# Optimization experiments

Hardware: AMD Instinct MI355X
Metric: run time of the kernel (lower is better)

Reference implementation:

```python
import jax, jax.numpy as jnp
import numpy as np

D = 1024
H = 16
DK = D // H
SCALE = 1.0 / jnp.sqrt(jnp.float32(DK))


def setup_inputs() -> dict:
    key0 = jax.random.key(0)
    ks = jax.random.split(key0, 11)
    B, S = 2, 2048
    std = 1.0 / np.sqrt(D)
    inp = {
        "query": jax.random.normal(ks[0], (B, S, D), jnp.float32),
        "key": jax.random.normal(ks[1], (B, S, D), jnp.float32),
        "value": jax.random.normal(ks[2], (B, S, D), jnp.float32),
        "wq": jax.random.normal(ks[3], (D, D), jnp.float32) * std,
        "bq": jax.random.normal(ks[4], (D,), jnp.float32) * std,
        "wk": jax.random.normal(ks[5], (D, D), jnp.float32) * std,
        "bk": jax.random.normal(ks[6], (D,), jnp.float32) * std,
        "wv": jax.random.normal(ks[7], (D, D), jnp.float32) * std,
        "bv": jax.random.normal(ks[8], (D,), jnp.float32) * std,
        "wo": jax.random.normal(ks[9], (D, D), jnp.float32) * std,
        "bo": jax.random.normal(ks[10], (D,), jnp.float32) * std,
    }
    return inp


def _split_heads(x):
    # [B,S,D] -> [B,H,S,dk]
    B, S, _ = x.shape
    return x.reshape(B, S, H, DK).transpose(0, 2, 1, 3)


def reference(query, key, value, wq, bq, wk, bk, wv, bv, wo, bo):
    B, S, _ = query.shape
    # Linear projections (torch nn.Linear: x @ W^T + b)
    q = _split_heads(query @ wq.T + bq)
    k = _split_heads(key @ wk.T + bk)
    v = _split_heads(value @ wv.T + bv)
    # Scaled dot-product attention scores [B,H,S,S]
    scores = jnp.einsum("bhqd,bhkd->bhqk", q * SCALE, k)
    attention = jax.nn.softmax(scores, axis=-1)
    # Dropout in eval mode == identity
    out = jnp.einsum("bhqk,bhkd->bhqd", attention, v)
    out = out.transpose(0, 2, 1, 3).reshape(B, S, D)
    out = out @ wo.T + bo
    return out, attention
```

## Files before the change

### kernel.cpp

```cpp
#include <hip/hip_runtime.h>
#include <stdint.h>

typedef __attribute__((ext_vector_type(4))) float f32x4;
typedef __attribute__((ext_vector_type(8))) short short8;
typedef __attribute__((ext_vector_type(2))) unsigned int u32x2;

#define MFMA16(a, b, c) __builtin_amdgcn_mfma_f32_16x16x32_bf16((a), (b), (c), 0, 0, 0)
#define EXP2(x) __builtin_amdgcn_exp2f(x)
#define LOG2(x) __builtin_amdgcn_logf(x)

__device__ __forceinline__ unsigned short f2bf(float f) {
  unsigned int x = __float_as_uint(f);
  return (unsigned short)((x + 0x7fffu + ((x >> 16) & 1u)) >> 16);
}

__device__ __forceinline__ unsigned int cvtpk(float lo, float hi) {
  unsigned int d;
  asm("v_cvt_pk_bf16_f32 %0, %1, %2" : "=v"(d) : "v"(lo), "v"(hi));
  return d;
}

__device__ __forceinline__ void gl2lds16(const void* g, void* l) {
  __builtin_amdgcn_global_load_lds((const __attribute__((address_space(1))) void*)g,
                                   (__attribute__((address_space(3))) void*)l, 16, 0, 0);
}

__device__ __forceinline__ void load8cv(const float* __restrict__ s, void* d) {
  const f32x4* p = (const f32x4*)s;
  f32x4 a = p[0], b = p[1];
  short8 t;
  t[0] = (short)f2bf(a[0]); t[1] = (short)f2bf(a[1]);
  t[2] = (short)f2bf(a[2]); t[3] = (short)f2bf(a[3]);
  t[4] = (short)f2bf(b[0]); t[5] = (short)f2bf(b[1]);
  t[6] = (short)f2bf(b[2]); t[7] = (short)f2bf(b[3]);
  *(short8*)d = t;
}

#define BAR_V4 asm volatile("s_waitcnt vmcnt(4)\ns_barrier" ::: "memory")
#define BAR_V8 asm volatile("s_waitcnt vmcnt(8)\ns_barrier" ::: "memory")
#define BAR_V0 asm volatile("s_waitcnt vmcnt(0)\ns_barrier" ::: "memory")
#define BAR_RAW asm volatile("s_barrier" ::: "memory")

__global__ __launch_bounds__(256) void cast_weights(const float* __restrict__ wq,
                                                    const float* __restrict__ wk,
                                                    const float* __restrict__ wv,
                                                    const float* __restrict__ wo,
                                                    unsigned short* __restrict__ dst) {
  int i = blockIdx.x * 256 + threadIdx.x;
  int which = i >> 17;
  int off = (i & 131071) * 8;
  const float* src = which == 0 ? wq : which == 1 ? wk : which == 2 ? wv : wo;
  load8cv(src + off, dst + (size_t)which * 1048576 + off);
}

__global__ __launch_bounds__(256) void qkv_proj(const float* __restrict__ q_in,
                                                const float* __restrict__ k_in,
                                                const float* __restrict__ v_in,
                                                const unsigned short* __restrict__ W16,
                                                const float* __restrict__ bq,
                                                const float* __restrict__ bk,
                                                const float* __restrict__ bv,
                                                unsigned short* __restrict__ Q16,
                                                unsigned short* __restrict__ K16,
                                                unsigned short* __restrict__ V16) {
  const int z = blockIdx.z;
  const float* A = z == 0 ? q_in : z == 1 ? k_in : v_in;
  const unsigned short* Bt = W16 + (size_t)z * 1048576;
  const float* bias = z == 0 ? bq : z == 1 ? bk : bv;
  unsigned short* C = z == 0 ? Q16 : z == 1 ? K16 : V16;
  const float oscale = z == 0 ? 0.18033688f : 1.0f;
  const int K = 1024, N = 1024;

  __shared__ __align__(16) char lds[32768];
  char* As = lds;
  char* Bs = lds + 16384;
  const int tid = threadIdx.x;
  const int lane = tid & 63;
  const int wv = tid >> 6;
  const int g = lane >> 4, r = lane & 15;
  const int wm = wv >> 1, wn = wv & 1;
  const int m0 = blockIdx.y * 128, n0 = blockIdx.x * 128;

  f32x4 acc[4][4];
#pragma unroll
  for (int m = 0; m < 4; ++m)
#pragma unroll
    for (int n = 0; n < 4; ++n) acc[m][n] = (f32x4){0.f, 0.f, 0.f, 0.f};

  for (int k0 = 0; k0 < K; k0 += 64) {
    __syncthreads();
#pragma unroll
    for (int i = 0; i < 4; ++i) {
      int c = (wv * 4 + i) * 64 + lane;
      int row = c >> 3;
      gl2lds16(Bt + (size_t)(n0 + row) * K + k0 + (c & 7) * 8, Bs + (wv * 4 + i) * 1024);
    }
#pragma unroll
    for (int i = 0; i < 4; ++i) {
      int c = tid + i * 256;
      int row = c >> 3, e = (c & 7) * 8;
      load8cv(A + (size_t)(m0 + row) * K + k0 + e, As + c * 16);
    }
    __syncthreads();
#pragma unroll
    for (int kk = 0; kk < 2; ++kk) {
      short8 af[4], bfr[4];
#pragma unroll
      for (int m = 0; m < 4; ++m)
        af[m] = *(const short8*)(As + (wm * 64 + m * 16 + r) * 128 + kk * 64 + g * 16);
#pragma unroll
      for (int n = 0; n < 4; ++n)
        bfr[n] = *(const short8*)(Bs + (wn * 64 + n * 16 + r) * 128 + kk * 64 + g * 16);
#pragma unroll
      for (int m = 0; m < 4; ++m)
#pragma unroll
        for (int n = 0; n < 4; ++n) acc[m][n] = MFMA16(af[m], bfr[n], acc[m][n]);
    }
  }

#pragma unroll
  for (int n = 0; n < 4; ++n) {
    int col = n0 + wn * 64 + n * 16 + r;
    float bv_ = bias[col];
#pragma unroll
    for (int m = 0; m < 4; ++m)
#pragma unroll
      for (int i = 0; i < 4; ++i) {
        int rowg = m0 + wm * 64 + m * 16 + 4 * g + i;
        C[(size_t)rowg * N + col] = f2bf((acc[m][n][i] + bv_) * oscale);
      }
  }
}

__global__ __launch_bounds__(256) void o_proj(const unsigned short* __restrict__ A,
                                              const unsigned short* __restrict__ Bt,
                                              const float* __restrict__ bias,
                                              float* __restrict__ C) {
  const int K = 1024, N = 1024;
  __shared__ __align__(16) char lds[24576];
  char* As = lds;
  char* Bs = lds + 16384;
  const int tid = threadIdx.x;
  const int lane = tid & 63;
  const int wv = tid >> 6;
  const int g = lane >> 4, r = lane & 15;
  const int wm = wv >> 1, wn = wv & 1;
  const int m0 = blockIdx.y * 128, n0 = blockIdx.x * 64;

  f32x4 acc[4][2];
#pragma unroll
  for (int m = 0; m < 4; ++m)
#pragma unroll
    for (int n = 0; n < 2; ++n) acc[m][n] = (f32x4){0.f, 0.f, 0.f, 0.f};

  for (int k0 = 0; k0 < K; k0 += 64) {
    __syncthreads();
#pragma unroll
    for (int i = 0; i < 2; ++i) {
      int c = (wv * 2 + i) * 64 + lane;
      int row = c >> 3;
      gl2lds16(Bt + (size_t)(n0 + row) * K + k0 + (c & 7) * 8, Bs + (wv * 2 + i) * 1024);
    }
#pragma unroll
    for (int i = 0; i < 4; ++i) {
      int c = (wv * 4 + i) * 64 + lane;
      int row = c >> 3;
      gl2lds16(A + (size_t)(m0 + row) * K + k0 + (c & 7) * 8, As + (wv * 4 + i) * 1024);
    }
    __syncthreads();
#pragma unroll
    for (int kk = 0; kk < 2; ++kk) {
      short8 af[4], bfr[2];
#pragma unroll
      for (int m = 0; m < 4; ++m)
        af[m] = *(const short8*)(As + (wm * 64 + m * 16 + r) * 128 + kk * 64 + g * 16);
#pragma unroll
      for (int n = 0; n < 2; ++n)
        bfr[n] = *(const short8*)(Bs + (wn * 32 + n * 16 + r) * 128 + kk * 64 + g * 16);
#pragma unroll
      for (int m = 0; m < 4; ++m)
#pragma unroll
        for (int n = 0; n < 2; ++n) acc[m][n] = MFMA16(af[m], bfr[n], acc[m][n]);
    }
  }

#pragma unroll
  for (int n = 0; n < 2; ++n) {
    int col = n0 + wn * 32 + n * 16 + r;
    float bv_ = bias[col];
#pragma unroll
    for (int m = 0; m < 4; ++m)
#pragma unroll
      for (int i = 0; i < 4; ++i) {
        int rowg = m0 + wm * 64 + m * 16 + 4 * g + i;
        C[(size_t)rowg * N + col] = acc[m][n][i] + bv_;
      }
  }
}

__global__ __launch_bounds__(256) void transpose_v(const unsigned short* __restrict__ V,
                                                   unsigned short* __restrict__ Vt) {
  int t = blockIdx.x * 256 + threadIdx.x;
  int d = t & 63;
  int sc = (t >> 6) & 255;
  int bh = t >> 14;
  int b = bh >> 4, h = bh & 15;
  unsigned short vals[8];
#pragma unroll
  for (int j = 0; j < 8; ++j)
    vals[j] = V[(size_t)(b * 2048 + sc * 8 + j) * 1024 + h * 64 + d];
  *(short8*)&Vt[((size_t)bh * 64 + d) * 2048 + sc * 8] = *(short8*)vals;
}

__global__ __launch_bounds__(256, 4) void attn_fused(const unsigned short* __restrict__ Q,
                                                     const unsigned short* __restrict__ K,
                                                     const unsigned short* __restrict__ Vt,
                                                     float* __restrict__ attn,
                                                     unsigned short* __restrict__ O) {
  __shared__ __align__(16) char lds[32768];
  const int tid = threadIdx.x;
  const int lane = tid & 63;
  const int wv = tid >> 6;
  const int g = lane >> 4, r = lane & 15;
  int nb = (blockIdx.x & 7) * 128 + (blockIdx.x >> 3);
  const int qt = nb & 31, bh = nb >> 5, h = bh & 15, b = bh >> 4;
  const int qloc = qt * 64 + wv * 16;
  const int qrow0 = b * 2048 + qloc;
  const unsigned short* Kbh = K + (size_t)b * 2048 * 1024 + h * 64;
  const unsigned short* Vbh = Vt + (size_t)bh * 64 * 2048;
  float* attn_bh = attn + (size_t)bh * 2048 * 2048;

  short8 qf[2];
#pragma unroll
  for (int kk = 0; kk < 2; ++kk)
    qf[kk] = *(const short8*)&Q[(size_t)(qrow0 + r) * 1024 + h * 64 + kk * 32 + g * 8];

#define P1_ISSUE(bb, ktt)                                                      \
  do {                                                                         \
    _Pragma("unroll") for (int i_ = 0; i_ < 4; ++i_) {                         \
      int c_ = (wv * 4 + i_) * 64 + lane;                                      \
      int kr_ = c_ >> 3;                                                       \
      int scb_ = ((c_ & 7) * 16) ^ ((kr_ & 7) << 4);                           \
      gl2lds16(Kbh + (size_t)((ktt) + kr_) * 1024 + (scb_ >> 1),               \
               (bb) + (wv * 4 + i_) * 1024);                                   \
    }                                                                          \
  } while (0)
#define P2_ISSUE(bb, ktt)                                                      \
  do {                                                                         \
    _Pragma("unroll") for (int i_ = 0; i_ < 4; ++i_) {                         \
      int c_ = (wv * 4 + i_) * 64 + lane;                                      \
      int kr_ = (c_ >> 3) & 63;                                                \
      int scb_ = ((c_ & 7) * 16) ^ ((kr_ & 7) << 4);                           \
      const unsigned short* src_ =                                             \
          (c_ < 512) ? (Kbh + (size_t)((ktt) + kr_) * 1024 + (scb_ >> 1))      \
                     : (Vbh + (size_t)kr_ * 2048 + (ktt) + (scb_ >> 1));       \
      gl2lds16(src_, (bb) + (wv * 4 + i_) * 1024);                             \
    }                                                                          \
  } while (0)

  float lrow = 0.f;
  int cur = 0;
  P1_ISSUE(lds, 0);
  for (int t = 0; t < 16; ++t) {
    char* bcur = lds + (cur << 14);
    char* bnxt = lds + ((cur ^ 1) << 14);
    if (t < 15) {
      P1_ISSUE(bnxt, (t + 1) * 128);
      BAR_V4;
    } else {
      BAR_V0;
    }
#pragma unroll
    for (int ct = 0; ct < 8; ++ct) {
      int row = ct * 16 + r;
      int sw = (row & 7) << 4;
      short8 kf0 = *(const short8*)(bcur + ((row * 128 + g * 16) ^ sw));
      short8 kf1 = *(const short8*)(bcur + ((row * 128 + 64 + g * 16) ^ sw));
      f32x4 s = (f32x4){0.f, 0.f, 0.f, 0.f};
      s = MFMA16(kf0, qf[0], s);
      s = MFMA16(kf1, qf[1], s);
      lrow += (EXP2(s[0]) + EXP2(s[1])) + (EXP2(s[2]) + EXP2(s[3]));
    }
    BAR_RAW;
    cur ^= 1;
  }
  lrow += __shfl_xor(lrow, 16);
  lrow += __shfl_xor(lrow, 32);
  const float negml = -LOG2(lrow);
  const f32x4 cinit = (f32x4){negml, negml, negml, negml};

  f32x4 oacc[4];
#pragma unroll
  for (int i = 0; i < 4; ++i) oacc[i] = (f32x4){0.f, 0.f, 0.f, 0.f};

  float* arow = attn_bh + (size_t)(qloc + r) * 2048 + 4 * g;
  cur = 0;
  P2_ISSUE(lds, 0);
  for (int t = 0; t < 32; ++t) {
    char* bcur = lds + (cur << 14);
    char* bnxt = lds + ((cur ^ 1) << 14);
    int kt = t * 64;
    if (t < 31) {
      P2_ISSUE(bnxt, kt + 64);
      if (t == 0) {
        BAR_V4;
      } else {
        BAR_V8;
      }
    } else {
      BAR_V0;
    }
    unsigned w[4][2];
#pragma unroll
    for (int ct = 0; ct < 4; ++ct) {
      int row = ct * 16 + r;
      int sw = (row & 7) << 4;
      short8 kf0 = *(const short8*)(bcur + ((row * 128 + g * 16) ^ sw));
      short8 kf1 = *(const short8*)(bcur + ((row * 128 + 64 + g * 16) ^ sw));
      f32x4 s = MFMA16(kf0, qf[0], cinit);
      s = MFMA16(kf1, qf[1], s);
      f32x4 p;
      p[0] = EXP2(s[0]); p[1] = EXP2(s[1]);
      p[2] = EXP2(s[2]); p[3] = EXP2(s[3]);
      __builtin_nontemporal_store(p, (f32x4*)(arow + kt + 16 * ct));
      w[ct][0] = cvtpk(p[0], p[1]);
      w[ct][1] = cvtpk(p[2], p[3]);
    }
    __builtin_amdgcn_s_setprio(1);
#pragma unroll
    for (int kk2 = 0; kk2 < 2; ++kk2) {
      unsigned x0 = w[2 * kk2][0], y0 = w[2 * kk2 + 1][0];
      unsigned x1 = w[2 * kk2][1], y1 = w[2 * kk2 + 1][1];
      asm("v_permlane32_swap_b32 %0, %1" : "+v"(x0), "+v"(y0));
      asm("v_permlane16_swap_b32 %0, %1" : "+v"(x0), "+v"(y0));
      asm("v_permlane32_swap_b32 %0, %1" : "+v"(x1), "+v"(y1));
      asm("v_permlane16_swap_b32 %0, %1" : "+v"(x1), "+v"(y1));
      union { unsigned u[4]; short8 v8; } pau;
      pau.u[0] = x0; pau.u[1] = x1; pau.u[2] = y0; pau.u[3] = y1;
      short8 pa = pau.v8;
#pragma unroll
      for (int ct2 = 0; ct2 < 4; ++ct2) {
        int vrow = ct2 * 16 + r;
        short8 vf = *(const short8*)(bcur + 8192 +
                                     ((vrow * 128 + kk2 * 64 + g * 16) ^ ((vrow & 7) << 4)));
        oacc[ct2] = MFMA16(pa, vf, oacc[ct2]);
      }
    }
    __builtin_amdgcn_s_setprio(0);
    BAR_RAW;
    cur ^= 1;
  }
#pragma unroll
  for (int ct2 = 0; ct2 < 4; ++ct2)
#pragma unroll
    for (int i = 0; i < 4; ++i)
      O[(size_t)(qrow0 + 4 * g + i) * 1024 + h * 64 + ct2 * 16 + r] = f2bf(oacc[ct2][i]);
#undef P1_ISSUE
#undef P2_ISSUE
}

extern "C" void kernel_launch(void* const* d_in, const int* in_sizes, int n_in,
                              void* d_out, int out_size, void* d_ws, size_t ws_size,
                              hipStream_t stream) {
  const float* q_in = (const float*)d_in[0];
  const float* k_in = (const float*)d_in[1];
  const float* v_in = (const float*)d_in[2];
  const float* wq = (const float*)d_in[3];
  const float* bq = (const float*)d_in[4];
  const float* wk = (const float*)d_in[5];
  const float* bk = (const float*)d_in[6];
  const float* wv = (const float*)d_in[7];
  const float* bv = (const float*)d_in[8];
  const float* wo = (const float*)d_in[9];
  const float* bo = (const float*)d_in[10];

  char* ws = (char*)d_ws;
  const size_t MB8 = 8ull * 1024 * 1024;
  unsigned short* W16 = (unsigned short*)(ws);
  unsigned short* Q16 = (unsigned short*)(ws + MB8);
  unsigned short* K16 = (unsigned short*)(ws + 2 * MB8);
  unsigned short* V16 = (unsigned short*)(ws + 3 * MB8);
  unsigned short* Vt  = (unsigned short*)(ws + 4 * MB8);
  unsigned short* O16 = (unsigned short*)(ws + 3 * MB8);

  float* out = (float*)d_out;
  float* attn = out + 4194304ull;

  dim3 blk(256);
  cast_weights<<<dim3(2048), blk, 0, stream>>>(wq, wk, wv, wo, W16);
  qkv_proj<<<dim3(8, 32, 3), blk, 0, stream>>>(q_in, k_in, v_in, W16, bq, bk, bv, Q16, K16, V16);
  transpose_v<<<dim3(2048), blk, 0, stream>>>(V16, Vt);
  attn_fused<<<dim3(1024), blk, 0, stream>>>(Q16, K16, Vt, attn, O16);
  o_proj<<<dim3(16, 32), blk, 0, stream>>>(O16, W16 + 3145728, bo, out);
}
```

Measured before the change: 290.3 us.

## Pre-cast activations to bf16 and restructure attention loop barriers

A merged cast kernel now converts the fp32 query/key/value inputs to bf16 along with the weights. The QKV projection then streams its A tiles straight into LDS with global_load_lds instead of converting per tile, which removes redundant fp32 loads and conversions across the 8 column blocks. The attention loops also change from issue-then-wait plus a trailing barrier to wait-then-issue with a single barrier per step, cutting one barrier per iteration. The trade-offs are an extra activation round trip through workspace memory and less prefetch overlap in phase one, since it now waits for vmcnt(0).

```diff
diff --git a/kernel.cpp b/kernel.cpp
--- a/kernel.cpp
+++ b/kernel.cpp
@@ -3,7 +3,6 @@
 
 typedef __attribute__((ext_vector_type(4))) float f32x4;
 typedef __attribute__((ext_vector_type(8))) short short8;
-typedef __attribute__((ext_vector_type(2))) unsigned int u32x2;
 
 #define MFMA16(a, b, c) __builtin_amdgcn_mfma_f32_16x16x32_bf16((a), (b), (c), 0, 0, 0)
 #define EXP2(x) __builtin_amdgcn_exp2f(x)
@@ -36,26 +35,39 @@
   *(short8*)d = t;
 }
 
-#define BAR_V4 asm volatile("s_waitcnt vmcnt(4)\ns_barrier" ::: "memory")
-#define BAR_V8 asm volatile("s_waitcnt vmcnt(8)\ns_barrier" ::: "memory")
-#define BAR_V0 asm volatile("s_waitcnt vmcnt(0)\ns_barrier" ::: "memory")
-#define BAR_RAW asm volatile("s_barrier" ::: "memory")
-
-__global__ __launch_bounds__(256) void cast_weights(const float* __restrict__ wq,
-                                                    const float* __restrict__ wk,
-                                                    const float* __restrict__ wv,
-                                                    const float* __restrict__ wo,
-                                                    unsigned short* __restrict__ dst) {
-  int i = blockIdx.x * 256 + threadIdx.x;
-  int which = i >> 17;
-  int off = (i & 131071) * 8;
-  const float* src = which == 0 ? wq : which == 1 ? wk : which == 2 ? wv : wo;
-  load8cv(src + off, dst + (size_t)which * 1048576 + off);
-}
-
-__global__ __launch_bounds__(256) void qkv_proj(const float* __restrict__ q_in,
+#define ENT_V0 asm volatile("s_waitcnt vmcnt(0)\ns_barrier" ::: "memory")
+#define ENT_V4 asm volatile("s_waitcnt vmcnt(4)\ns_barrier" ::: "memory")
+
+__global__ __launch_bounds__(256) void cast_all(const float* __restrict__ wq,
+                                                const float* __restrict__ wk,
+                                                const float* __restrict__ wv,
+                                                const float* __restrict__ wo,
+                                                const float* __restrict__ q_in,
                                                 const float* __restrict__ k_in,
                                                 const float* __restrict__ v_in,
+                                                unsigned short* __restrict__ W16,
+                                                unsigned short* __restrict__ Qin,
+                                                unsigned short* __restrict__ Kin,
+                                                unsigned short* __restrict__ Vin) {
+  int i = blockIdx.x * 256 + threadIdx.x;
+  if (i < 524288) {
+    int which = i >> 17;
+    int off = (i & 131071) * 8;
+    const float* src = which == 0 ? wq : which == 1 ? wk : which == 2 ? wv : wo;
+    load8cv(src + off, W16 + (size_t)which * 1048576 + off);
+  } else {
+    int j = i - 524288;
+    int which = j >> 19;
+    int off = (j & 524287) * 8;
+    const float* src = which == 0 ? q_in : which == 1 ? k_in : v_in;
+    unsigned short* dst = which == 0 ? Qin : which == 1 ? Kin : Vin;
+    load8cv(src + off, dst + off);
+  }
+}
+
+__global__ __launch_bounds__(256) void qkv_proj(const unsigned short* __restrict__ Qin,
+                                                const unsigned short* __restrict__ Kin,
+                                                const unsigned short* __restrict__ Vin,
                                                 const unsigned short* __restrict__ W16,
                                                 const float* __restrict__ bq,
                                                 const float* __restrict__ bk,
@@ -64,7 +76,7 @@
                                                 unsigned short* __restrict__ K16,
                                                 unsigned short* __restrict__ V16) {
   const int z = blockIdx.z;
-  const float* A = z == 0 ? q_in : z == 1 ? k_in : v_in;
+  const unsigned short* A = z == 0 ? Qin : z == 1 ? Kin : Vin;
   const unsigned short* Bt = W16 + (size_t)z * 1048576;
   const float* bias = z == 0 ? bq : z == 1 ? bk : bv;
   unsigned short* C = z == 0 ? Q16 : z == 1 ? K16 : V16;
@@ -97,9 +109,9 @@
     }
 #pragma unroll
     for (int i = 0; i < 4; ++i) {
-      int c = tid + i * 256;
-      int row = c >> 3, e = (c & 7) * 8;
-      load8cv(A + (size_t)(m0 + row) * K + k0 + e, As + c * 16);
+      int c = (wv * 4 + i) * 64 + lane;
+      int row = c >> 3;
+      gl2lds16(A + (size_t)(m0 + row) * K + k0 + (c & 7) * 8, As + (wv * 4 + i) * 1024);
     }
     __syncthreads();
 #pragma unroll
@@ -263,13 +275,8 @@
   P1_ISSUE(lds, 0);
   for (int t = 0; t < 16; ++t) {
     char* bcur = lds + (cur << 14);
-    char* bnxt = lds + ((cur ^ 1) << 14);
-    if (t < 15) {
-      P1_ISSUE(bnxt, (t + 1) * 128);
-      BAR_V4;
-    } else {
-      BAR_V0;
-    }
+    ENT_V0;
+    if (t < 15) P1_ISSUE(lds + ((cur ^ 1) << 14), (t + 1) * 128);
 #pragma unroll
     for (int ct = 0; ct < 8; ++ct) {
       int row = ct * 16 + r;
@@ -281,7 +288,6 @@
       s = MFMA16(kf1, qf[1], s);
       lrow += (EXP2(s[0]) + EXP2(s[1])) + (EXP2(s[2]) + EXP2(s[3]));
     }
-    BAR_RAW;
     cur ^= 1;
   }
   lrow += __shfl_xor(lrow, 16);
@@ -298,18 +304,13 @@
   P2_ISSUE(lds, 0);
   for (int t = 0; t < 32; ++t) {
     char* bcur = lds + (cur << 14);
-    char* bnxt = lds + ((cur ^ 1) << 14);
     int kt = t * 64;
-    if (t < 31) {
-      P2_ISSUE(bnxt, kt + 64);
-      if (t == 0) {
-        BAR_V4;
-      } else {
-        BAR_V8;
-      }
+    if (t == 0) {
+      ENT_V0;
     } else {
-      BAR_V0;
-    }
+      ENT_V4;
+    }
+    if (t < 31) P2_ISSUE(lds + ((cur ^ 1) << 14), kt + 64);
     unsigned w[4][2];
 #pragma unroll
     for (int ct = 0; ct < 4; ++ct) {
@@ -347,7 +348,6 @@
       }
     }
     __builtin_amdgcn_s_setprio(0);
-    BAR_RAW;
     cur ^= 1;
   }
 #pragma unroll
@@ -377,18 +377,21 @@
   char* ws = (char*)d_ws;
   const size_t MB8 = 8ull * 1024 * 1024;
   unsigned short* W16 = (unsigned short*)(ws);
-  unsigned short* Q16 = (unsigned short*)(ws + MB8);
-  unsigned short* K16 = (unsigned short*)(ws + 2 * MB8);
-  unsigned short* V16 = (unsigned short*)(ws + 3 * MB8);
-  unsigned short* Vt  = (unsigned short*)(ws + 4 * MB8);
-  unsigned short* O16 = (unsigned short*)(ws + 3 * MB8);
+  unsigned short* Qin = (unsigned short*)(ws + MB8);
+  unsigned short* Kin = (unsigned short*)(ws + 2 * MB8);
+  unsigned short* Vin = (unsigned short*)(ws + 3 * MB8);
+  unsigned short* Q16 = (unsigned short*)(ws + 4 * MB8);
+  unsigned short* K16 = (unsigned short*)(ws + 5 * MB8);
+  unsigned short* V16 = (unsigned short*)(ws + 6 * MB8);
+  unsigned short* Vt  = (unsigned short*)(ws + 7 * MB8);
+  unsigned short* O16 = (unsigned short*)(ws + 6 * MB8);
 
   float* out = (float*)d_out;
   float* attn = out + 4194304ull;
 
   dim3 blk(256);
-  cast_weights<<<dim3(2048), blk, 0, stream>>>(wq, wk, wv, wo, W16);
-  qkv_proj<<<dim3(8, 32, 3), blk, 0, stream>>>(q_in, k_in, v_in, W16, bq, bk, bv, Q16, K16, V16);
+  cast_all<<<dim3(8192), blk, 0, stream>>>(wq, wk, wv, wo, q_in, k_in, v_in, W16, Qin, Kin, Vin);
+  qkv_proj<<<dim3(8, 32, 3), blk, 0, stream>>>(Qin, Kin, Vin, W16, bq, bk, bv, Q16, K16, V16);
   transpose_v<<<dim3(2048), blk, 0, stream>>>(V16, Vt);
   attn_fused<<<dim3(1024), blk, 0, stream>>>(Q16, K16, Vt, attn, O16);
   o_proj<<<dim3(16, 32), blk, 0, stream>>>(O16, W16 + 3145728, bo, out);
```

Result: faster. 269.4 us (median of 2 runs) (-7.2%).
